# Performance work log

Hardware: AMD Instinct MI355X
Metric: run time of the kernel (lower is better)

Reference implementation:

```python
import jax, jax.numpy as jnp
from jax import lax
import numpy as np

B, T, E, D, OUT = 512, 128, 256, 256, 1

def setup_inputs() -> dict:
    key = jax.random.key(0)
    ks = jax.random.split(key, 16)
    s = lambda *sh: 1.0 / np.sqrt(sh[-1])
    inp = {
        "input_encoded": jax.random.normal(ks[0], (B, T, E), jnp.float32),
        "y_history": jax.random.normal(ks[1], (B, T, OUT), jnp.float32),
        # attn_layer: Linear(2D+E -> E), Tanh, Linear(E -> 1). Stored input-major [in, out].
        "aW1": jax.random.normal(ks[2], (2 * D + E, E), jnp.float32) * (1.0 / np.sqrt(2 * D + E)),
        "ab1": jnp.zeros((E,), jnp.float32),
        "aW2": jax.random.normal(ks[3], (E, 1), jnp.float32) * (1.0 / np.sqrt(E)),
        "ab2": jnp.zeros((1,), jnp.float32),
        # LSTM cell (input_size=OUT, hidden=D), torch gate order i,f,g,o; weights [4D, in]
        "Wih": jax.random.normal(ks[4], (4 * D, OUT), jnp.float32) * (1.0 / np.sqrt(D)),
        "Whh": jax.random.normal(ks[5], (4 * D, D), jnp.float32) * (1.0 / np.sqrt(D)),
        "bih": jnp.zeros((4 * D,), jnp.float32),
        "bhh": jnp.zeros((4 * D,), jnp.float32),
        # fc: Linear(E+OUT -> OUT), weight init normal_() per source
        "fcW": jax.random.normal(ks[6], (OUT, E + OUT), jnp.float32),
        "fcb": jnp.zeros((OUT,), jnp.float32),
        # fc_final: Linear(D+E -> OUT)
        "ffW": jax.random.normal(ks[7], (OUT, D + E), jnp.float32) * (1.0 / np.sqrt(D + E)),
        "ffb": jnp.zeros((OUT,), jnp.float32),
    }
    return inp

def _decoder(input_encoded, y_history, aW1, ab1, aW2, ab2, Wih, Whh, bih, bhh, fcW, fcb, ffW, ffb):
    b, t, e = input_encoded.shape
    d = Whh.shape[1]
    # Precompute the encoder part of the attention projection once: [b, t, e_hid]
    enc_proj = jnp.einsum('bte,ef->btf', input_encoded, aW1[2 * d:])

    def step(carry, y_t):
        h, c, _ = carry                                  # h,c: [b, d]
        hc = jnp.concatenate([h, c], axis=-1)            # [b, 2d]
        z = jnp.tanh(jnp.einsum('bk,kf->bf', hc, aW1[:2 * d])[:, None, :] + enc_proj + ab1)
        scores = jnp.einsum('btf,f->bt', z, aW2[:, 0]) + ab2[0]
        attn = jax.nn.softmax(scores, axis=1)            # [b, t]
        ctx = jnp.einsum('bt,bte->be', attn, input_encoded)  # [b, e]
        y_tilde = jnp.concatenate([ctx, y_t], axis=-1) @ fcW.T + fcb  # [b, out]
        gates = y_tilde @ Wih.T + h @ Whh.T + (bih + bhh)  # [b, 4d]
        i, f, g, o = jnp.split(gates, 4, axis=-1)
        c2 = jax.nn.sigmoid(f) * c + jax.nn.sigmoid(i) * jnp.tanh(g)
        h2 = jax.nn.sigmoid(o) * jnp.tanh(c2)
        return (h2, c2, ctx), None

    init = (jnp.zeros((b, d), input_encoded.dtype),
            jnp.zeros((b, d), input_encoded.dtype),
            jnp.zeros((b, e), input_encoded.dtype))
    (h, c, ctx), _ = lax.scan(step, init, jnp.swapaxes(y_history, 0, 1))
    return jnp.concatenate([h, ctx], axis=-1) @ ffW.T + ffb  # [b, out]

def reference(input_encoded, y_history, aW1, ab1, aW2, ab2, Wih, Whh, bih, bhh, fcW, fcb, ffW, ffb):
    return _decoder(input_encoded, y_history, aW1, ab1, aW2, ab2, Wih, Whh, bih, bhh, fcW, fcb, ffW, ffb)
```

## Files before the change

### kernel.cpp

```cpp
#include <hip/hip_runtime.h>


#define BB 512
#define TT 128
#define EE 256
#define DD 256
#define NB 2
#define NTHR 1024

typedef _Float16 h2 __attribute__((ext_vector_type(2)));
typedef _Float16 h8 __attribute__((ext_vector_type(8)));

#if defined(__has_builtin)
#if __has_builtin(__builtin_amdgcn_fdot2)
#define HAS_FDOT2 1
#endif
#endif

#ifdef HAS_FDOT2
#define FDOT2(a, b, c) __builtin_amdgcn_fdot2(__builtin_bit_cast(h2, (a)), __builtin_bit_cast(h2, (b)), (c), false)
#else
static __device__ __forceinline__ float FDOT2(unsigned int a, unsigned int b, float c) {
    h2 x = __builtin_bit_cast(h2, a), y = __builtin_bit_cast(h2, b);
    return c + (float)x[0] * (float)y[0] + (float)x[1] * (float)y[1];
}
#endif

static __device__ __forceinline__ float dot8u4(uint4 w, uint4 h, float acc) {
    acc = FDOT2(w.x, h.x, acc);
    acc = FDOT2(w.y, h.y, acc);
    acc = FDOT2(w.z, h.z, acc);
    acc = FDOT2(w.w, h.w, acc);
    return acc;
}
static __device__ __forceinline__ unsigned int pkh(float a, float b) {
    union { _Float16 h; unsigned short s; } ua, ub;
    ua.h = (_Float16)a; ub.h = (_Float16)b;
    return (unsigned int)ua.s | ((unsigned int)ub.s << 16);
}
__device__ __forceinline__ float ftanh(float x) {
    return 1.f - 2.f * __builtin_amdgcn_rcpf(__expf(2.f * x) + 1.f);
}
__device__ __forceinline__ float fsig(float x) {
    return __builtin_amdgcn_rcpf(1.f + __expf(-x));
}

__global__ __launch_bounds__(256) void k_pack(const float* __restrict__ aW1,
                                              const float* __restrict__ Whh,
                                              const float* __restrict__ bih,
                                              const float* __restrict__ bhh,
                                              _Float16* __restrict__ aW1h,
                                              _Float16* __restrict__ WhhH,
                                              float* __restrict__ bias) {
    int bid = blockIdx.x, tid = threadIdx.x;
    if (bid < 512) {
        int o = bid * 256 + tid;
        int g = o >> 11, f = (o >> 3) & 255, j = o & 7;
        aW1h[o] = (_Float16)aW1[(g * 8 + j) * EE + f];
    } else if (bid < 1536) {
        int o = (bid - 512) * 256 + tid;
        int i = o >> 13, jj = (o >> 3) & 1023, m = o & 7;
        WhhH[o] = (_Float16)Whh[jj * DD + i * 8 + m];
    } else {
        int j = (bid - 1536) * 256 + tid;
        bias[j] = bih[j] + bhh[j];
    }
}

__global__ __launch_bounds__(256) void k_encproj(const float* __restrict__ ie,
                                                 const float* __restrict__ aW1,
                                                 const float* __restrict__ fcW,
                                                 const float* __restrict__ ffW,
                                                 _Float16* __restrict__ ep,
                                                 float* __restrict__ iefc,
                                                 float* __restrict__ ieff) {
    __shared__ float a[32][EE];
    int row0 = blockIdx.x * 32;
    int tid = threadIdx.x;
    for (int r = 0; r < 32; ++r)
        a[r][tid] = ie[(size_t)(row0 + r) * EE + tid];
    __syncthreads();
    float acc[32];
    #pragma unroll
    for (int r = 0; r < 32; ++r) acc[r] = 0.f;
    const float* wenc = aW1 + 512 * EE;
    for (int e = 0; e < EE; e += 4) {
        float w0 = wenc[(e + 0) * EE + tid];
        float w1 = wenc[(e + 1) * EE + tid];
        float w2 = wenc[(e + 2) * EE + tid];
        float w3 = wenc[(e + 3) * EE + tid];
        #pragma unroll
        for (int r = 0; r < 32; ++r) {
            float4 av = *(const float4*)&a[r][e];
            acc[r] += av.x * w0 + av.y * w1 + av.z * w2 + av.w * w3;
        }
    }
    for (int r = 0; r < 32; ++r)
        ep[(size_t)(row0 + r) * EE + tid] = (_Float16)acc[r];

    int wave = tid >> 6, lane = tid & 63;
    float4 f1 = *(const float4*)&fcW[lane * 4];
    float4 f2 = *(const float4*)&ffW[EE + lane * 4];
    #pragma unroll
    for (int rr = 0; rr < 8; ++rr) {
        int r = wave * 8 + rr;
        float4 v = *(const float4*)&a[r][lane * 4];
        float p1 = v.x * f1.x + v.y * f1.y + v.z * f1.z + v.w * f1.w;
        float p2 = v.x * f2.x + v.y * f2.y + v.z * f2.z + v.w * f2.w;
        #pragma unroll
        for (int off = 1; off <= 32; off <<= 1) {
            p1 += __shfl_xor(p1, off);
            p2 += __shfl_xor(p2, off);
        }
        if (lane == 0) {
            iefc[row0 + r] = p1;
            ieff[row0 + r] = p2;
        }
    }
}

__global__ __launch_bounds__(NTHR) void k_main(
    const _Float16* __restrict__ ep, const float* __restrict__ yh,
    const _Float16* __restrict__ aW1h, const _Float16* __restrict__ WhhH,
    const float* __restrict__ bias_, const float* __restrict__ ab1,
    const float* __restrict__ aW2, const float* __restrict__ Wih,
    const float* __restrict__ fcW, const float* __restrict__ fcb,
    const float* __restrict__ ffW, const float* __restrict__ ffb,
    const float* __restrict__ iefc, const float* __restrict__ ieff,
    float* __restrict__ out) {
    __shared__ unsigned int s_hc16[NB][2][128];
    __shared__ float s_qp[2][NB][EE];
    __shared__ float s_sc[NB * TT];
    __shared__ float s_g[NB][4 * DD];
    __shared__ float s_wih[4 * DD];
    __shared__ float s_iefc[NB][TT];
    __shared__ float s_ieff[NB][TT];
    __shared__ float s_yh[NB][TT];
    __shared__ float s_yt[NB];
    __shared__ float s_ofs[NB];

    const int tid = threadIdx.x;
    const int wave = tid >> 6, lane = tid & 63;
    const int b0 = blockIdx.x * NB;

    for (int i = tid; i < 4 * DD; i += NTHR) s_wih[i] = Wih[i];
    for (int i = tid; i < NB * TT; i += NTHR) {
        int b = i >> 7, t = i & 127;
        s_iefc[b][t] = iefc[(b0 + b) * TT + t];
        s_ieff[b][t] = ieff[(b0 + b) * TT + t];
        s_yh[b][t]   = yh[(size_t)(b0 + b) * TT + t];
    }
    for (int i = tid; i < NB * 2 * 128; i += NTHR) (&s_hc16[0][0][0])[i] = 0u;

    const int qf = tid & 255, qkh = (tid >> 8) & 1, qb = tid >> 9;
    const float qinit = qkh ? 0.f : ab1[qf];
    const uint4* qW = (const uint4*)aW1h + ((size_t)(qkh * 32) * 256 + qf);
    const int qperm = 32 * 0 + (qf >> 3) + 32 * (qf & 7) - 0;

    const uint4* wP = (const uint4*)WhhH + tid;
    const float biasv = bias_[tid];

    const int l5 = lane & 31;
    const int rsub = wave * 2 + (lane >> 5);
    const int e0 = l5 * 8;
    float tw2[8]; float sw2 = 0.f;
    #pragma unroll
    for (int j = 0; j < 8; ++j) { float w = aW2[e0 + j]; tw2[j] = 2.f * w; sw2 += w; }

    const float fcw256 = fcW[256], fcb0 = fcb[0], ffb0 = ffb[0];
    float c_reg = 0.f;

    __syncthreads();

    for (int t = 0; t < TT; ++t) {
        float qa = qinit;
        float g0 = biasv, g1 = biasv;
        #pragma unroll 8
        for (int i = 0; i < 32; ++i) {
            uint4 wv = qW[(size_t)i * 256];
            uint4 hv = *(const uint4*)&s_hc16[qb][qkh][i * 4];
            qa = dot8u4(wv, hv, qa);
            uint4 gw = wP[(size_t)i * 1024];
            uint4 h0 = *(const uint4*)&s_hc16[0][0][i * 4];
            uint4 h1 = *(const uint4*)&s_hc16[1][0][i * 4];
            g0 = dot8u4(gw, h0, g0);
            g1 = dot8u4(gw, h1, g1);
        }
        s_qp[qkh][qb][qperm] = qa;
        s_g[0][tid] = g0;
        s_g[1][tid] = g1;
        __syncthreads();

        #pragma unroll
        for (int b = 0; b < NB; ++b) {
            float qs[8];
            #pragma unroll
            for (int j = 0; j < 8; ++j)
                qs[j] = 2.f * (s_qp[0][b][l5 + 32 * j] + s_qp[1][b][l5 + 32 * j]);
            const _Float16* eph = ep + (size_t)(b0 + b) * TT * EE + e0;
            #pragma unroll
            for (int sw = 0; sw < 4; ++sw) {
                int tt2 = sw * 32 + rsub;
                h8 xv = *(const h8*)(eph + (size_t)tt2 * EE);
                float s = sw2;
                #pragma unroll
                for (int j = 0; j < 8; ++j) {
                    float e = __expf(__fmaf_rn((float)xv[j], 2.f, qs[j]));
                    s = __fmaf_rn(-tw2[j], __builtin_amdgcn_rcpf(e + 1.f), s);
                }
                #pragma unroll
                for (int off = 1; off <= 16; off <<= 1) s += __shfl_xor(s, off);
                if (l5 == 0) s_sc[b * TT + tt2] = s;
            }
        }
        __syncthreads();

        if ((wave & 7) == 0) {
            int b = wave >> 3;
            float v0 = s_sc[b * TT + lane], v1 = s_sc[b * TT + 64 + lane];
            float m = fmaxf(v0, v1);
            #pragma unroll
            for (int off = 1; off <= 32; off <<= 1) m = fmaxf(m, __shfl_xor(m, off));
            float x0 = __expf(v0 - m), x1 = __expf(v1 - m);
            float ss = x0 + x1;
            #pragma unroll
            for (int off = 1; off <= 32; off <<= 1) ss += __shfl_xor(ss, off);
            float inv = __builtin_amdgcn_rcpf(ss);
            float a0 = x0 * inv, a1 = x1 * inv;
            float p  = a0 * s_iefc[b][lane] + a1 * s_iefc[b][64 + lane];
            float pf = (t == TT - 1) ? (a0 * s_ieff[b][lane] + a1 * s_ieff[b][64 + lane]) : 0.f;
            #pragma unroll
            for (int off = 1; off <= 32; off <<= 1) {
                p  += __shfl_xor(p, off);
                pf += __shfl_xor(pf, off);
            }
            if (lane == 0) {
                s_yt[b] = p + s_yh[b][t] * fcw256 + fcb0;
                if (t == TT - 1) s_ofs[b] = pf;
            }
        }
        __syncthreads();

        if (tid < NB * DD) {
            int b = tid >> 8, d = tid & 255;
            float yt = s_yt[b];
            float gi = s_g[b][d]          + yt * s_wih[d];
            float gf = s_g[b][DD + d]     + yt * s_wih[DD + d];
            float gg = s_g[b][2 * DD + d] + yt * s_wih[2 * DD + d];
            float go = s_g[b][3 * DD + d] + yt * s_wih[3 * DD + d];
            float c2 = fsig(gf) * c_reg + fsig(gi) * ftanh(gg);
            c_reg = c2;
            float hn = fsig(go) * ftanh(c2);
            float hO = __shfl_xor(hn, 1);
            float cO = __shfl_xor(c2, 1);
            if (!(d & 1)) {
                s_hc16[b][0][d >> 1] = pkh(hn, hO);
                s_hc16[b][1][d >> 1] = pkh(c2, cO);
            }
        }
        __syncthreads();
    }

    if ((wave & 7) == 0) {
        int b = wave >> 3;
        unsigned int p0 = s_hc16[b][0][lane * 2];
        unsigned int p1 = s_hc16[b][0][lane * 2 + 1];
        h2 ha = __builtin_bit_cast(h2, p0), hb = __builtin_bit_cast(h2, p1);
        float4 w = *(const float4*)&ffW[lane * 4];
        float p = (float)ha[0] * w.x + (float)ha[1] * w.y
                + (float)hb[0] * w.z + (float)hb[1] * w.w;
        #pragma unroll
        for (int off = 1; off <= 32; off <<= 1) p += __shfl_xor(p, off);
        if (lane == 0) out[b0 + b] = p + s_ofs[b] + ffb0;
    }
}

extern "C" void kernel_launch(void* const* d_in, const int* in_sizes, int n_in,
                              void* d_out, int out_size, void* d_ws, size_t ws_size,
                              hipStream_t stream) {
    const float* ie  = (const float*)d_in[0];
    const float* yh  = (const float*)d_in[1];
    const float* aW1 = (const float*)d_in[2];
    const float* ab1 = (const float*)d_in[3];
    const float* aW2 = (const float*)d_in[4];
    const float* Wih = (const float*)d_in[6];
    const float* Whh = (const float*)d_in[7];
    const float* bih = (const float*)d_in[8];
    const float* bhh = (const float*)d_in[9];
    const float* fcW = (const float*)d_in[10];
    const float* fcb = (const float*)d_in[11];
    const float* ffW = (const float*)d_in[12];
    const float* ffb = (const float*)d_in[13];
    float* out = (float*)d_out;

    _Float16* ep   = (_Float16*)d_ws;
    _Float16* aW1h = ep + (size_t)BB * TT * EE;
    _Float16* WhhH = aW1h + 512 * EE;
    float* bias = (float*)(WhhH + 262144);
    float* iefc = bias + 1024;
    float* ieff = iefc + BB * TT;

    k_pack<<<1540, 256, 0, stream>>>(aW1, Whh, bih, bhh, aW1h, WhhH, bias);
    k_encproj<<<2048, 256, 0, stream>>>(ie, aW1, fcW, ffW, ep, iefc, ieff);
    k_main<<<BB / NB, NTHR, 0, stream>>>(ep, yh, aW1h, WhhH, bias, ab1, aW2,
                                         Wih, fcW, fcb, ffW, ffb, iefc, ieff, out);
}
```

Measured before the change: 2.060 ms.

## Split block into attention and gate warp groups and overlap Whh matvec with scoring

The block is split into two roles. The first 512 threads compute the attention query for both batches and then the attention scores. The other 512 threads compute the Whh gate matvec, split across the two phases so it runs alongside the score computation. The softmax, context reduction and LSTM update are merged into one phase run by the first group, with every wave redundantly reducing y_tilde instead of going through shared memory. This removes one barrier per step. The risk is load imbalance between the groups, plus more redundant shuffle reductions.

```diff
diff --git a/kernel.cpp b/kernel.cpp
--- a/kernel.cpp
+++ b/kernel.cpp
@@ -136,12 +136,11 @@
     __shared__ float s_iefc[NB][TT];
     __shared__ float s_ieff[NB][TT];
     __shared__ float s_yh[NB][TT];
-    __shared__ float s_yt[NB];
-    __shared__ float s_ofs[NB];
 
     const int tid = threadIdx.x;
     const int wave = tid >> 6, lane = tid & 63;
     const int b0 = blockIdx.x * NB;
+    const bool isQ = tid < 512;
 
     for (int i = tid; i < 4 * DD; i += NTHR) s_wih[i] = Wih[i];
     for (int i = tid; i < NB * TT; i += NTHR) {
@@ -152,16 +151,18 @@
     }
     for (int i = tid; i < NB * 2 * 128; i += NTHR) (&s_hc16[0][0][0])[i] = 0u;
 
-    const int qf = tid & 255, qkh = (tid >> 8) & 1, qb = tid >> 9;
+    const int qf = tid & 255, qkh = (tid >> 8) & 1;
     const float qinit = qkh ? 0.f : ab1[qf];
     const uint4* qW = (const uint4*)aW1h + ((size_t)(qkh * 32) * 256 + qf);
-    const int qperm = 32 * 0 + (qf >> 3) + 32 * (qf & 7) - 0;
-
-    const uint4* wP = (const uint4*)WhhH + tid;
-    const float biasv = bias_[tid];
+    const int qperm = 32 * (qf & 7) + (qf >> 3);
+
+    const int gt = tid & 511;
+    const uint4* wPa = (const uint4*)WhhH + gt;
+    const uint4* wPb = (const uint4*)WhhH + gt + 512;
+    const float bias_a = bias_[gt], bias_b = bias_[gt + 512];
 
     const int l5 = lane & 31;
-    const int rsub = wave * 2 + (lane >> 5);
+    const int rsub = (wave & 7) * 2 + (lane >> 5);
     const int e0 = l5 * 8;
     float tw2[8]; float sw2 = 0.f;
     #pragma unroll
@@ -169,54 +170,84 @@
 
     const float fcw256 = fcW[256], fcb0 = fcb[0], ffb0 = ffb[0];
     float c_reg = 0.f;
+    float ofs_reg = 0.f;
+    float g_a0 = 0.f, g_a1 = 0.f, g_b0 = 0.f, g_b1 = 0.f;
 
     __syncthreads();
 
     for (int t = 0; t < TT; ++t) {
-        float qa = qinit;
-        float g0 = biasv, g1 = biasv;
-        #pragma unroll 8
-        for (int i = 0; i < 32; ++i) {
-            uint4 wv = qW[(size_t)i * 256];
-            uint4 hv = *(const uint4*)&s_hc16[qb][qkh][i * 4];
-            qa = dot8u4(wv, hv, qa);
-            uint4 gw = wP[(size_t)i * 1024];
-            uint4 h0 = *(const uint4*)&s_hc16[0][0][i * 4];
-            uint4 h1 = *(const uint4*)&s_hc16[1][0][i * 4];
-            g0 = dot8u4(gw, h0, g0);
-            g1 = dot8u4(gw, h1, g1);
-        }
-        s_qp[qkh][qb][qperm] = qa;
-        s_g[0][tid] = g0;
-        s_g[1][tid] = g1;
+        if (isQ) {
+            float qa0 = qinit, qa1 = qinit;
+            #pragma unroll 8
+            for (int i = 0; i < 32; ++i) {
+                uint4 wv = qW[(size_t)i * 256];
+                uint4 h0 = *(const uint4*)&s_hc16[0][qkh][i * 4];
+                uint4 h1 = *(const uint4*)&s_hc16[1][qkh][i * 4];
+                qa0 = dot8u4(wv, h0, qa0);
+                qa1 = dot8u4(wv, h1, qa1);
+            }
+            s_qp[qkh][0][qperm] = qa0;
+            s_qp[qkh][1][qperm] = qa1;
+        } else {
+            g_a0 = bias_a; g_a1 = bias_a; g_b0 = bias_b; g_b1 = bias_b;
+            #pragma unroll 8
+            for (int i = 0; i < 16; ++i) {
+                uint4 wa = wPa[(size_t)i * 1024];
+                uint4 wb = wPb[(size_t)i * 1024];
+                uint4 h0 = *(const uint4*)&s_hc16[0][0][i * 4];
+                uint4 h1 = *(const uint4*)&s_hc16[1][0][i * 4];
+                g_a0 = dot8u4(wa, h0, g_a0);
+                g_a1 = dot8u4(wa, h1, g_a1);
+                g_b0 = dot8u4(wb, h0, g_b0);
+                g_b1 = dot8u4(wb, h1, g_b1);
+            }
+        }
         __syncthreads();
 
-        #pragma unroll
-        for (int b = 0; b < NB; ++b) {
-            float qs[8];
+        if (isQ) {
             #pragma unroll
-            for (int j = 0; j < 8; ++j)
-                qs[j] = 2.f * (s_qp[0][b][l5 + 32 * j] + s_qp[1][b][l5 + 32 * j]);
-            const _Float16* eph = ep + (size_t)(b0 + b) * TT * EE + e0;
-            #pragma unroll
-            for (int sw = 0; sw < 4; ++sw) {
-                int tt2 = sw * 32 + rsub;
-                h8 xv = *(const h8*)(eph + (size_t)tt2 * EE);
-                float s = sw2;
+            for (int b = 0; b < NB; ++b) {
+                float qs[8];
                 #pragma unroll
-                for (int j = 0; j < 8; ++j) {
-                    float e = __expf(__fmaf_rn((float)xv[j], 2.f, qs[j]));
-                    s = __fmaf_rn(-tw2[j], __builtin_amdgcn_rcpf(e + 1.f), s);
+                for (int j = 0; j < 8; ++j)
+                    qs[j] = 2.f * (s_qp[0][b][l5 + 32 * j] + s_qp[1][b][l5 + 32 * j]);
+                const _Float16* eph = ep + (size_t)(b0 + b) * TT * EE + e0;
+                #pragma unroll
+                for (int sw = 0; sw < 8; ++sw) {
+                    int tt2 = sw * 16 + rsub;
+                    h8 xv = *(const h8*)(eph + (size_t)tt2 * EE);
+                    float s = sw2;
+                    #pragma unroll
+                    for (int j = 0; j < 8; ++j) {
+                        float e = __expf(__fmaf_rn((float)xv[j], 2.f, qs[j]));
+                        s = __fmaf_rn(-tw2[j], __builtin_amdgcn_rcpf(e + 1.f), s);
+                    }
+                    #pragma unroll
+                    for (int off = 1; off <= 16; off <<= 1) s += __shfl_xor(s, off);
+                    if (l5 == 0) s_sc[b * TT + tt2] = s;
                 }
-                #pragma unroll
-                for (int off = 1; off <= 16; off <<= 1) s += __shfl_xor(s, off);
-                if (l5 == 0) s_sc[b * TT + tt2] = s;
-            }
+            }
+        } else {
+            #pragma unroll 8
+            for (int i = 16; i < 32; ++i) {
+                uint4 wa = wPa[(size_t)i * 1024];
+                uint4 wb = wPb[(size_t)i * 1024];
+                uint4 h0 = *(const uint4*)&s_hc16[0][0][i * 4];
+                uint4 h1 = *(const uint4*)&s_hc16[1][0][i * 4];
+                g_a0 = dot8u4(wa, h0, g_a0);
+                g_a1 = dot8u4(wa, h1, g_a1);
+                g_b0 = dot8u4(wb, h0, g_b0);
+                g_b1 = dot8u4(wb, h1, g_b1);
+            }
+            s_g[0][gt]       = g_a0;
+            s_g[1][gt]       = g_a1;
+            s_g[0][gt + 512] = g_b0;
+            s_g[1][gt + 512] = g_b1;
         }
         __syncthreads();
 
-        if ((wave & 7) == 0) {
-            int b = wave >> 3;
+        if (isQ) {
+            int b = tid >> 8, d = tid & 255;
             float v0 = s_sc[b * TT + lane], v1 = s_sc[b * TT + 64 + lane];
             float m = fmaxf(v0, v1);
             #pragma unroll
@@ -227,23 +258,16 @@
             for (int off = 1; off <= 32; off <<= 1) ss += __shfl_xor(ss, off);
             float inv = __builtin_amdgcn_rcpf(ss);
             float a0 = x0 * inv, a1 = x1 * inv;
-            float p  = a0 * s_iefc[b][lane] + a1 * s_iefc[b][64 + lane];
-            float pf = (t == TT - 1) ? (a0 * s_ieff[b][lane] + a1 * s_ieff[b][64 + lane]) : 0.f;
+            float p = a0 * s_iefc[b][lane] + a1 * s_iefc[b][64 + lane];
             #pragma unroll
-            for (int off = 1; off <= 32; off <<= 1) {
-                p  += __shfl_xor(p, off);
-                pf += __shfl_xor(pf, off);
-            }
-            if (lane == 0) {
-                s_yt[b] = p + s_yh[b][t] * fcw256 + fcb0;
-                if (t == TT - 1) s_ofs[b] = pf;
-            }
-        }
-        __syncthreads();
-
-        if (tid < NB * DD) {
-            int b = tid >> 8, d = tid & 255;
-            float yt = s_yt[b];
+            for (int off = 1; off <= 32; off <<= 1) p += __shfl_xor(p, off);
+            float yt = p + s_yh[b][t] * fcw256 + fcb0;
+            if (t == TT - 1) {
+                float pf = a0 * s_ieff[b][lane] + a1 * s_ieff[b][64 + lane];
+                #pragma unroll
+                for (int off = 1; off <= 32; off <<= 1) pf += __shfl_xor(pf, off);
+                ofs_reg = pf;
+            }
             float gi = s_g[b][d]          + yt * s_wih[d];
             float gf = s_g[b][DD + d]     + yt * s_wih[DD + d];
             float gg = s_g[b][2 * DD + d] + yt * s_wih[2 * DD + d];
@@ -261,8 +285,8 @@
         __syncthreads();
     }
 
-    if ((wave & 7) == 0) {
-        int b = wave >> 3;
+    if (wave == 0 || wave == 4) {
+        int b = wave >> 2;
         unsigned int p0 = s_hc16[b][0][lane * 2];
         unsigned int p1 = s_hc16[b][0][lane * 2 + 1];
         h2 ha = __builtin_bit_cast(h2, p0), hb = __builtin_bit_cast(h2, p1);
@@ -271,7 +295,7 @@
                 + (float)hb[0] * w.z + (float)hb[1] * w.w;
         #pragma unroll
         for (int off = 1; off <= 32; off <<= 1) p += __shfl_xor(p, off);
-        if (lane == 0) out[b0 + b] = p + s_ofs[b] + ffb0;
+        if (lane == 0) out[b0 + b] = p + ofs_reg + ffb0;
     }
 }
 
```

After: 2.621 ms. +27.2%, slower.
